# Performance work log

Hardware: AMD Instinct MI355X
Metric: run time of the kernel (lower is better)

The kernel has to match this reference:

```python
import jax, jax.numpy as jnp
import numpy as np

N, E = 50000, 800000
DIN, DH, DOUT = 128, 128, 64


def setup_inputs() -> dict:
    key = jax.random.key(0)
    ks = jax.random.split(key, 18)
    s = 0.05
    inp = {
        "x": jax.random.normal(ks[0], (N, DIN), dtype=jnp.float32),
        "edge_index": jax.random.randint(ks[1], (2, E), 0, N, dtype=jnp.int64),
        # conv1 MLP: Linear(DIN,DH), Linear(DH,DH)
        "c1_w1": jax.random.normal(ks[2], (DIN, DH), dtype=jnp.float32) * s,
        "c1_b1": jax.random.normal(ks[3], (DH,), dtype=jnp.float32) * s,
        "c1_w2": jax.random.normal(ks[4], (DH, DH), dtype=jnp.float32) * s,
        "c1_b2": jax.random.normal(ks[5], (DH,), dtype=jnp.float32) * s,
        # conv2 MLP
        "c2_w1": jax.random.normal(ks[6], (DH, DH), dtype=jnp.float32) * s,
        "c2_b1": jax.random.normal(ks[7], (DH,), dtype=jnp.float32) * s,
        "c2_w2": jax.random.normal(ks[8], (DH, DH), dtype=jnp.float32) * s,
        "c2_b2": jax.random.normal(ks[9], (DH,), dtype=jnp.float32) * s,
        # conv3 MLP
        "c3_w1": jax.random.normal(ks[10], (DH, DH), dtype=jnp.float32) * s,
        "c3_b1": jax.random.normal(ks[11], (DH,), dtype=jnp.float32) * s,
        "c3_w2": jax.random.normal(ks[12], (DH, DH), dtype=jnp.float32) * s,
        "c3_b2": jax.random.normal(ks[13], (DH,), dtype=jnp.float32) * s,
        # output head
        "lin1_w": jax.random.normal(ks[14], (DH, DH), dtype=jnp.float32) * s,
        "lin1_b": jax.random.normal(ks[15], (DH,), dtype=jnp.float32) * s,
        "lin2_w": jax.random.normal(ks[16], (DH, DOUT), dtype=jnp.float32) * s,
        "lin2_b": jax.random.normal(ks[17], (DOUT,), dtype=jnp.float32) * s,
    }
    return inp


def _gin_conv(h, src, dst, w1, b1, w2, b2):
    # PyG GINConv, eps=0: MLP((1+eps)*x + sum_{j->i} x_j)
    agg = jax.ops.segment_sum(h[src], dst, num_segments=h.shape[0])  # [N, D]
    z = h + agg
    z = jax.nn.relu(z @ w1 + b1)
    return jax.nn.relu(z @ w2 + b2)


def reference(x, edge_index, c1_w1, c1_b1, c1_w2, c1_b2,
              c2_w1, c2_b1, c2_w2, c2_b2,
              c3_w1, c3_b1, c3_w2, c3_b2,
              lin1_w, lin1_b, lin2_w, lin2_b):
    src, dst = edge_index[0], edge_index[1]
    h = _gin_conv(x, src, dst, c1_w1, c1_b1, c1_w2, c1_b2)
    h = jax.nn.relu(h)  # redundant after MLP ReLU, but faithful to source
    h = _gin_conv(h, src, dst, c2_w1, c2_b1, c2_w2, c2_b2)
    h = jax.nn.relu(h)
    h = _gin_conv(h, src, dst, c3_w1, c3_b1, c3_w2, c3_b2)
    h = jax.nn.relu(h @ lin1_w + lin1_b)
    return h @ lin2_w + lin2_b  # [N, DOUT]
```

## Files before the change

### kernel.cpp

```cpp
#include <hip/hip_runtime.h>
#include <hip/hip_bf16.h>

typedef __attribute__((ext_vector_type(8))) short bf16x8;
typedef __attribute__((ext_vector_type(4))) float f32x4;

#define DH 128
#define DOUT 64

static __device__ __forceinline__ unsigned short f2bf(float f) {
    __hip_bfloat16 h = __float2bfloat16(f);
    return *(unsigned short*)&h;
}
static __device__ __forceinline__ void accI(float& a0, float& a1, unsigned u, float s) {
    int lo = (int)(signed char)(u & 0xffu);
    int hi = (int)(signed char)(u >> 8);
    a0 += s * (float)lo;
    a1 += s * (float)hi;
}


struct WPrep {
    const float* src[8];
    unsigned short* dst[8];
};

__global__ void prep_conv_kernel(const float* __restrict__ x,
                                 char* __restrict__ xq, float* __restrict__ sx,
                                 char* __restrict__ hAq, float* __restrict__ sA,
                                 char* __restrict__ hBq, float* __restrict__ sB,
                                 int nA, WPrep p,
                                 int* __restrict__ cnt, int* __restrict__ rank,
                                 const int* __restrict__ dstv, int E, int N_) {
    int id = blockIdx.x * blockDim.x + threadIdx.x;
    if (id < nA) {
        float4 v = ((const float4*)x)[id];
        float m = fmaxf(fmaxf(fabsf(v.x), fabsf(v.y)), fmaxf(fabsf(v.z), fabsf(v.w)));
#pragma unroll
        for (int d = 16; d >= 1; d >>= 1) m = fmaxf(m, __shfl_xor(m, d));
        float inv = m > 0.f ? 127.f / m : 0.f;
        int q0 = __float2int_rn(v.x * inv);
        int q1 = __float2int_rn(v.y * inv);
        int q2 = __float2int_rn(v.z * inv);
        int q3 = __float2int_rn(v.w * inv);
        unsigned pk = (q0 & 0xff) | ((q1 & 0xff) << 8) | ((q2 & 0xff) << 16) | ((q3 & 0xff) << 24);
        ((unsigned*)xq)[id] = pk;
        if ((id & 31) == 0) sx[id >> 5] = m * (1.f / 127.f);
        return;
    }
    id -= nA;
    if (id < 7 * 16384 + 8192) {
        int m, off;
        if (id < 7 * 16384) { m = id >> 14; off = id & 16383; }
        else { m = 7; off = id - 7 * 16384; }
        int shift = (m == 7) ? 6 : 7;
        int nc = 1 << shift;
        int k = off >> shift;
        int n = off & (nc - 1);
        p.dst[m][n * 128 + k] = f2bf(p.src[m][off]);
        return;
    }
    id -= 7 * 16384 + 8192;
    if (id < 96) {
        int w = id >> 5, j = id & 31;
        unsigned* dst = (unsigned*)(w == 0 ? xq : (w == 1 ? hAq : hBq));
        dst[(size_t)N_ * 32 + j] = 0u;
        return;
    }
    id -= 96;
    if (id < 3) {
        (id == 0 ? sx : (id == 1 ? sA : sB))[N_] = 0.f;
        return;
    }
    id -= 3;
    if (id < E) {
        int d = dstv[id];
        if ((unsigned)d < (unsigned)N_) rank[id] = atomicAdd(&cnt[d], 1);
    }
}


__global__ void scan1_kernel(const int* __restrict__ cnt, int* __restrict__ rp_part,
                             int* __restrict__ bsum, int n) {
    __shared__ int s[256];
    int tid = threadIdx.x;
    int i = blockIdx.x * 256 + tid;
    int v = (i < n) ? ((cnt[i] + 7) & ~7) : 0;
    s[tid] = v;
    __syncthreads();
    for (int off = 1; off < 256; off <<= 1) {
        int t = (tid >= off) ? s[tid - off] : 0;
        __syncthreads();
        s[tid] += t;
        __syncthreads();
    }
    if (i <= n) rp_part[i] = s[tid] - v;
    if (tid == 255) bsum[blockIdx.x] = s[255];
}

__global__ void scan2_kernel(int* __restrict__ bsum, int nb) {
    __shared__ int s[256];
    int tid = threadIdx.x;
    int v = (tid < nb) ? bsum[tid] : 0;
    s[tid] = v;
    __syncthreads();
    for (int off = 1; off < 256; off <<= 1) {
        int t = (tid >= off) ? s[tid - off] : 0;
        __syncthreads();
        s[tid] += t;
        __syncthreads();
    }
    if (tid < nb) bsum[tid] = s[tid] - v;
}

__global__ void scan3_fill_kernel(const int* __restrict__ rp_part, const int* __restrict__ bsum,
                                  int* __restrict__ row_ptr,
                                  const int* __restrict__ src, const int* __restrict__ dst,
                                  const int* __restrict__ rank, const int* __restrict__ cnt,
                                  unsigned short* __restrict__ esrc,
                                  int n, int E) {
    int gid = blockIdx.x * blockDim.x + threadIdx.x;
    if (gid <= n) row_ptr[gid] = rp_part[gid] + bsum[gid >> 8];
    if (gid < n) {
        int st = rp_part[gid] + bsum[gid >> 8];
        int c = cnt[gid];
        int pe = (c + 7) & ~7;
        for (int j = c; j < pe; ++j) esrc[st + j] = (unsigned short)n;
    }
    if (gid < E) {
        int d = dst[gid];
        if ((unsigned)d < (unsigned)n)
            esrc[rp_part[d] + bsum[d >> 8] + rank[gid]] = (unsigned short)src[gid];
    }
}


template <bool HEAD>
__launch_bounds__(256, 6)
__global__ void layer_kernel(const char* __restrict__ hq, const float* __restrict__ sIn,
                             const int* __restrict__ rp,
                             const unsigned short* __restrict__ esrc,
                             const unsigned short* __restrict__ W1t,
                             const float* __restrict__ b1,
                             const unsigned short* __restrict__ W2t,
                             const float* __restrict__ b2,
                             const unsigned short* __restrict__ W3t,
                             const float* __restrict__ b3,
                             const unsigned short* __restrict__ W4t,
                             const float* __restrict__ b4,
                             char* __restrict__ outq, float* __restrict__ outs,
                             float* __restrict__ outp, int M) {
    constexpr int LDA = 128 + 8;
    constexpr int CAP = 1024;
    __shared__ __align__(16) unsigned short As[16][LDA];
    __shared__ __align__(16) unsigned short Zs[16][LDA];
    __shared__ __align__(16) int2 sIdx[CAP];

    int tid = threadIdx.x;
    int wave = __builtin_amdgcn_readfirstlane(tid >> 6);
    int lane = tid & 63;
    int row0 = blockIdx.x * 16;
    int nd0 = row0 + wave * 4;

    const char* hc = hq;
    unsigned voff = (unsigned)lane << 1;

    int wbv = rp[row0];
    int Cv = rp[min(row0 + 16, M)] - wbv;
    int wb = __builtin_amdgcn_readfirstlane(wbv);
    int C = __builtin_amdgcn_readfirstlane(Cv);

    int b[4], e[4];
#pragma unroll
    for (int i = 0; i < 4; ++i) {
        int ndc = min(nd0 + i, M);
        int nd1 = min(nd0 + i + 1, M);
        b[i] = rp[ndc] - wb;
        e[i] = rp[nd1] - wb;
    }

    float a0[4] = {0.f, 0.f, 0.f, 0.f}, a1[4] = {0.f, 0.f, 0.f, 0.f};

    for (int p0 = 0; p0 < C; p0 += CAP) {
        int cend = min(C, p0 + CAP);
        for (int i = tid; i < cend - p0; i += 256) {
            int id = esrc[wb + p0 + i];
            sIdx[i] = make_int2(id << 7, __float_as_int(sIn[id]));
        }
        __syncthreads();
#pragma unroll
        for (int i = 0; i < 4; ++i) {
            int nb = max(b[i], p0) - p0;
            int ne = min(e[i], cend) - p0;
            if (nb < ne) {
                int2 ia[8];
                unsigned ua[8];
#pragma unroll
                for (int t = 0; t < 8; ++t) ia[t] = sIdx[nb + t];
#pragma unroll
                for (int t = 0; t < 8; ++t)
                    ua[t] = *(const unsigned short*)(hc + (unsigned)ia[t].x + voff);
                for (int r = nb + 8; r < ne; r += 8) {
                    int2 ib[8];
                    unsigned ub[8];
#pragma unroll
                    for (int t = 0; t < 8; ++t) ib[t] = sIdx[r + t];
#pragma unroll
                    for (int t = 0; t < 8; ++t)
                        ub[t] = *(const unsigned short*)(hc + (unsigned)ib[t].x + voff);
#pragma unroll
                    for (int t = 0; t < 8; ++t) accI(a0[i], a1[i], ua[t], __int_as_float(ia[t].y));
#pragma unroll
                    for (int t = 0; t < 8; ++t) { ia[t] = ib[t]; ua[t] = ub[t]; }
                }
#pragma unroll
                for (int t = 0; t < 8; ++t) accI(a0[i], a1[i], ua[t], __int_as_float(ia[t].y));
            }
        }
        __syncthreads();
    }

#pragma unroll
    for (int i = 0; i < 4; ++i) {
        int ndc = min(nd0 + i, M);
        unsigned su = *(const unsigned short*)(hc + ((size_t)(unsigned)ndc << 7) + voff);
        accI(a0[i], a1[i], su, sIn[ndc]);
        unsigned pv = (unsigned)f2bf(a0[i]) | ((unsigned)f2bf(a1[i]) << 16);
        *(unsigned*)&As[wave * 4 + i][lane * 2] = pv;
    }
    __syncthreads();

    int quad = lane >> 4;
    int l16 = lane & 15;

    bf16x8 af[4];
#pragma unroll
    for (int kt = 0; kt < 4; ++kt)
        af[kt] = *(const bf16x8*)(&As[l16][kt * 32 + quad * 8]);
#pragma unroll
    for (int p = 0; p < 2; ++p) {
        int ncol = (wave * 2 + p) * 16 + l16;
        const unsigned short* wp = W1t + ncol * 128 + quad * 8;
        f32x4 a = {0.f, 0.f, 0.f, 0.f};
#pragma unroll
        for (int kt = 0; kt < 4; ++kt)
            a = __builtin_amdgcn_mfma_f32_16x16x32_bf16(
                af[kt], *(const bf16x8*)(wp + kt * 32), a, 0, 0, 0);
        float bs = b1[ncol];
#pragma unroll
        for (int r = 0; r < 4; ++r) {
            float v = a[r] + bs;
            if (v < 0.f) v = 0.f;
            Zs[quad * 4 + r][ncol] = f2bf(v);
        }
    }
    __syncthreads();

    bf16x8 zf[4];
#pragma unroll
    for (int kt = 0; kt < 4; ++kt)
        zf[kt] = *(const bf16x8*)(&Zs[l16][kt * 32 + quad * 8]);

    if (!HEAD) {
        __shared__ float Fs[16][132];
#pragma unroll
        for (int p = 0; p < 2; ++p) {
            int ncol = (wave * 2 + p) * 16 + l16;
            const unsigned short* wp = W2t + ncol * 128 + quad * 8;
            f32x4 a = {0.f, 0.f, 0.f, 0.f};
#pragma unroll
            for (int kt = 0; kt < 4; ++kt)
                a = __builtin_amdgcn_mfma_f32_16x16x32_bf16(
                    zf[kt], *(const bf16x8*)(wp + kt * 32), a, 0, 0, 0);
            float bs = b2[ncol];
#pragma unroll
            for (int r = 0; r < 4; ++r) {
                float v = a[r] + bs;
                if (v < 0.f) v = 0.f;
                Fs[quad * 4 + r][ncol] = v;
            }
        }
        __syncthreads();
        {
            int row = tid >> 4;
            int c0 = (tid & 15) * 8;
            float v8[8];
            float m = 0.f;
#pragma unroll
            for (int j = 0; j < 8; ++j) { v8[j] = Fs[row][c0 + j]; m = fmaxf(m, v8[j]); }
#pragma unroll
            for (int d = 8; d >= 1; d >>= 1) m = fmaxf(m, __shfl_xor(m, d));
            float inv = m > 0.f ? 127.f / m : 0.f;
            unsigned w0 = 0, w1 = 0;
#pragma unroll
            for (int j = 0; j < 4; ++j) {
                w0 |= (unsigned)(__float2int_rn(v8[j] * inv) & 0xff) << (8 * j);
                w1 |= (unsigned)(__float2int_rn(v8[4 + j] * inv) & 0xff) << (8 * j);
            }
            int grow = row0 + row;
            if (grow < M) {
                uint2 pk = make_uint2(w0, w1);
                ((uint2*)(outq + (size_t)grow * 128))[tid & 15] = pk;
                if ((tid & 15) == 0) outs[grow] = m * (1.f / 127.f);
            }
        }
    } else {
#pragma unroll
        for (int p = 0; p < 2; ++p) {
            int ncol = (wave * 2 + p) * 16 + l16;
            const unsigned short* wp = W2t + ncol * 128 + quad * 8;
            f32x4 a = {0.f, 0.f, 0.f, 0.f};
#pragma unroll
            for (int kt = 0; kt < 4; ++kt)
                a = __builtin_amdgcn_mfma_f32_16x16x32_bf16(
                    zf[kt], *(const bf16x8*)(wp + kt * 32), a, 0, 0, 0);
            float bs = b2[ncol];
#pragma unroll
            for (int r = 0; r < 4; ++r) {
                float v = a[r] + bs;
                if (v < 0.f) v = 0.f;
                As[quad * 4 + r][ncol] = f2bf(v);
            }
        }
        __syncthreads();
        bf16x8 hf[4];
#pragma unroll
        for (int kt = 0; kt < 4; ++kt)
            hf[kt] = *(const bf16x8*)(&As[l16][kt * 32 + quad * 8]);
#pragma unroll
        for (int p = 0; p < 2; ++p) {
            int ncol = (wave * 2 + p) * 16 + l16;
            const unsigned short* wp = W3t + ncol * 128 + quad * 8;
            f32x4 a = {0.f, 0.f, 0.f, 0.f};
#pragma unroll
            for (int kt = 0; kt < 4; ++kt)
                a = __builtin_amdgcn_mfma_f32_16x16x32_bf16(
                    hf[kt], *(const bf16x8*)(wp + kt * 32), a, 0, 0, 0);
            float bs = b3[ncol];
#pragma unroll
            for (int r = 0; r < 4; ++r) {
                float v = a[r] + bs;
                if (v < 0.f) v = 0.f;
                Zs[quad * 4 + r][ncol] = f2bf(v);
            }
        }
        __syncthreads();
        bf16x8 gf[4];
#pragma unroll
        for (int kt = 0; kt < 4; ++kt)
            gf[kt] = *(const bf16x8*)(&Zs[l16][kt * 32 + quad * 8]);
        {
            int ncol = wave * 16 + l16;
            const unsigned short* wp = W4t + ncol * 128 + quad * 8;
            f32x4 a = {0.f, 0.f, 0.f, 0.f};
#pragma unroll
            for (int kt = 0; kt < 4; ++kt)
                a = __builtin_amdgcn_mfma_f32_16x16x32_bf16(
                    gf[kt], *(const bf16x8*)(wp + kt * 32), a, 0, 0, 0);
            float bs = b4[ncol];
#pragma unroll
            for (int r = 0; r < 4; ++r) {
                int grow = row0 + quad * 4 + r;
                if (grow < M)
                    outp[(size_t)grow * 64 + ncol] = a[r] + bs;
            }
        }
    }
}


extern "C" void kernel_launch(void* const* d_in, const int* in_sizes, int n_in,
                              void* d_out, int out_size, void* d_ws, size_t ws_size,
                              hipStream_t stream) {
    const float* x = (const float*)d_in[0];
    const int* ei = (const int*)d_in[1];
    int N = in_sizes[0] / DH;
    int E = in_sizes[1] / 2;
    const int* src = ei;
    const int* dstv = ei + E;
    int Epad = E + 7 * N + 1024;

    char* ws = (char*)d_ws;
    size_t off = 0;
    auto alloc = [&](size_t bytes) -> void* {
        void* p = ws + off;
        off += (bytes + 255) & ~(size_t)255;
        return p;
    };
    char* xq  = (char*)alloc((size_t)(N + 1) * 128);
    char* hAq = (char*)alloc((size_t)(N + 1) * 128);
    char* hBq = (char*)alloc((size_t)(N + 1) * 128);
    float* sx = (float*)alloc((size_t)(N + 1) * 4);
    float* sA = (float*)alloc((size_t)(N + 1) * 4);
    float* sB = (float*)alloc((size_t)(N + 1) * 4);
    unsigned short* wt[8];
    for (int m = 0; m < 8; ++m) wt[m] = (unsigned short*)alloc(16384 * 2);
    int* cnt     = (int*)alloc((size_t)N * 4);
    int* rp_part = (int*)alloc((size_t)(N + 1) * 4);
    int* row_ptr = (int*)alloc((size_t)(N + 1) * 4);
    int* rank    = (int*)alloc((size_t)E * 4);
    int* bsum    = (int*)alloc(256 * 4);
    unsigned short* esrc = (unsigned short*)alloc((size_t)Epad * 2);

    WPrep wp;
    wp.src[0] = (const float*)d_in[2];
    wp.src[1] = (const float*)d_in[4];
    wp.src[2] = (const float*)d_in[6];
    wp.src[3] = (const float*)d_in[8];
    wp.src[4] = (const float*)d_in[10];
    wp.src[5] = (const float*)d_in[12];
    wp.src[6] = (const float*)d_in[14];
    wp.src[7] = (const float*)d_in[16];
    for (int m = 0; m < 8; ++m) wp.dst[m] = wt[m];

    hipMemsetAsync(cnt, 0, (size_t)N * 4, stream);

    int nA = N * 32;
    int conv_items = nA + 7 * 16384 + 8192 + 99 + E;
    prep_conv_kernel<<<(conv_items + 255) / 256, 256, 0, stream>>>(
        x, xq, sx, hAq, sA, hBq, sB, nA, wp, cnt, rank, dstv, E, N);

    int nb = (N + 1 + 255) / 256;
    int eb = (E + 255) / 256;
    scan1_kernel<<<nb, 256, 0, stream>>>(cnt, rp_part, bsum, N);
    scan2_kernel<<<1, 256, 0, stream>>>(bsum, nb);
    scan3_fill_kernel<<<eb, 256, 0, stream>>>(rp_part, bsum, row_ptr,
                                              src, dstv, rank, cnt, esrc, N, E);

    int gb = (N + 15) / 16;

    const float* c1b1 = (const float*)d_in[3];
    const float* c1b2 = (const float*)d_in[5];
    const float* c2b1 = (const float*)d_in[7];
    const float* c2b2 = (const float*)d_in[9];
    const float* c3b1 = (const float*)d_in[11];
    const float* c3b2 = (const float*)d_in[13];
    const float* l1b  = (const float*)d_in[15];
    const float* l2b  = (const float*)d_in[17];

    layer_kernel<false><<<gb, 256, 0, stream>>>(
        xq, sx, row_ptr, esrc, wt[0], c1b1, wt[1], c1b2,
        nullptr, nullptr, nullptr, nullptr, hAq, sA, nullptr, N);
    layer_kernel<false><<<gb, 256, 0, stream>>>(
        hAq, sA, row_ptr, esrc, wt[2], c2b1, wt[3], c2b2,
        nullptr, nullptr, nullptr, nullptr, hBq, sB, nullptr, N);
    layer_kernel<true><<<gb, 256, 0, stream>>>(
        hBq, sB, row_ptr, esrc, wt[4], c3b1, wt[5], c3b2,
        wt[6], l1b, wt[7], l2b, nullptr, nullptr, (float*)d_out, N);
}
```

Measured before the change: 311.1 us.

## Replace CSR build with per-block destination bins sorted in LDS

After: 335.8 us. 1.08x slower.

```diff
diff --git a/kernel.cpp b/kernel.cpp
--- a/kernel.cpp
+++ b/kernel.cpp
@@ -6,6 +6,7 @@
 
 #define DH 128
 #define DOUT 64
+#define BINCAP 1024
 
 static __device__ __forceinline__ unsigned short f2bf(float f) {
     __hip_bfloat16 h = __float2bfloat16(f);
@@ -29,8 +30,9 @@
                                  char* __restrict__ hAq, float* __restrict__ sA,
                                  char* __restrict__ hBq, float* __restrict__ sB,
                                  int nA, WPrep p,
-                                 int* __restrict__ cnt, int* __restrict__ rank,
-                                 const int* __restrict__ dstv, int E, int N_) {
+                                 int* __restrict__ bcnt, unsigned* __restrict__ binbuf,
+                                 const int* __restrict__ srcv, const int* __restrict__ dstv,
+                                 int E, int N_) {
     int id = blockIdx.x * blockDim.x + threadIdx.x;
     if (id < nA) {
         float4 v = ((const float4*)x)[id];
@@ -74,62 +76,13 @@
     id -= 3;
     if (id < E) {
         int d = dstv[id];
-        if ((unsigned)d < (unsigned)N_) rank[id] = atomicAdd(&cnt[d], 1);
-    }
-}
-
-
-__global__ void scan1_kernel(const int* __restrict__ cnt, int* __restrict__ rp_part,
-                             int* __restrict__ bsum, int n) {
-    __shared__ int s[256];
-    int tid = threadIdx.x;
-    int i = blockIdx.x * 256 + tid;
-    int v = (i < n) ? ((cnt[i] + 7) & ~7) : 0;
-    s[tid] = v;
-    __syncthreads();
-    for (int off = 1; off < 256; off <<= 1) {
-        int t = (tid >= off) ? s[tid - off] : 0;
-        __syncthreads();
-        s[tid] += t;
-        __syncthreads();
-    }
-    if (i <= n) rp_part[i] = s[tid] - v;
-    if (tid == 255) bsum[blockIdx.x] = s[255];
-}
-
-__global__ void scan2_kernel(int* __restrict__ bsum, int nb) {
-    __shared__ int s[256];
-    int tid = threadIdx.x;
-    int v = (tid < nb) ? bsum[tid] : 0;
-    s[tid] = v;
-    __syncthreads();
-    for (int off = 1; off < 256; off <<= 1) {
-        int t = (tid >= off) ? s[tid - off] : 0;
-        __syncthreads();
-        s[tid] += t;
-        __syncthreads();
-    }
-    if (tid < nb) bsum[tid] = s[tid] - v;
-}
-
-__global__ void scan3_fill_kernel(const int* __restrict__ rp_part, const int* __restrict__ bsum,
-                                  int* __restrict__ row_ptr,
-                                  const int* __restrict__ src, const int* __restrict__ dst,
-                                  const int* __restrict__ rank, const int* __restrict__ cnt,
-                                  unsigned short* __restrict__ esrc,
-                                  int n, int E) {
-    int gid = blockIdx.x * blockDim.x + threadIdx.x;
-    if (gid <= n) row_ptr[gid] = rp_part[gid] + bsum[gid >> 8];
-    if (gid < n) {
-        int st = rp_part[gid] + bsum[gid >> 8];
-        int c = cnt[gid];
-        int pe = (c + 7) & ~7;
-        for (int j = c; j < pe; ++j) esrc[st + j] = (unsigned short)n;
-    }
-    if (gid < E) {
-        int d = dst[gid];
-        if ((unsigned)d < (unsigned)n)
-            esrc[rp_part[d] + bsum[d >> 8] + rank[gid]] = (unsigned short)src[gid];
+        if ((unsigned)d < (unsigned)N_) {
+            int bin = d >> 4;
+            int pos = atomicAdd(&bcnt[bin], 1);
+            if (pos < BINCAP)
+                binbuf[(size_t)bin * BINCAP + pos] =
+                    (unsigned)srcv[id] | ((unsigned)(d & 15) << 16);
+        }
     }
 }
 
@@ -137,8 +90,7 @@
 template <bool HEAD>
 __launch_bounds__(256, 6)
 __global__ void layer_kernel(const char* __restrict__ hq, const float* __restrict__ sIn,
-                             const int* __restrict__ rp,
-                             const unsigned short* __restrict__ esrc,
+                             const int* __restrict__ bcnt, const unsigned* __restrict__ binbuf,
                              const unsigned short* __restrict__ W1t,
                              const float* __restrict__ b1,
                              const unsigned short* __restrict__ W2t,
@@ -150,10 +102,11 @@
                              char* __restrict__ outq, float* __restrict__ outs,
                              float* __restrict__ outp, int M) {
     constexpr int LDA = 128 + 8;
-    constexpr int CAP = 1024;
+    constexpr int SCAP = BINCAP + 16 * 8;
     __shared__ __align__(16) unsigned short As[16][LDA];
     __shared__ __align__(16) unsigned short Zs[16][LDA];
-    __shared__ __align__(16) int2 sIdx[CAP];
+    __shared__ __align__(16) int2 sIdx[SCAP];
+    __shared__ int nS[16], nE[16], nCur[16], CtotS;
 
     int tid = threadIdx.x;
     int wave = __builtin_amdgcn_readfirstlane(tid >> 6);
@@ -164,60 +117,77 @@
     const char* hc = hq;
     unsigned voff = (unsigned)lane << 1;
 
-    int wbv = rp[row0];
-    int Cv = rp[min(row0 + 16, M)] - wbv;
-    int wb = __builtin_amdgcn_readfirstlane(wbv);
-    int C = __builtin_amdgcn_readfirstlane(Cv);
+    int bin = blockIdx.x;
+    int C0 = min(bcnt[bin], BINCAP);
+    const unsigned* bb = binbuf + (size_t)bin * BINCAP;
+    if (tid < 16) nS[tid] = 0;
+    __syncthreads();
+    for (int i = tid; i < C0; i += 256) atomicAdd(&nS[(bb[i] >> 16) & 15], 1);
+    __syncthreads();
+    if (tid == 0) {
+        int acc = 0;
+#pragma unroll
+        for (int k = 0; k < 16; ++k) {
+            int c = nS[k];
+            nS[k] = acc; nCur[k] = acc;
+            acc += (c + 7) & ~7;
+            nE[k] = acc;
+        }
+        CtotS = acc;
+    }
+    __syncthreads();
+    int Ctot = __builtin_amdgcn_readfirstlane(CtotS);
+    int2 zent = make_int2(M << 7, 0);
+    for (int i = tid; i < Ctot; i += 256) sIdx[i] = zent;
+    __syncthreads();
+    for (int i = tid; i < C0; i += 256) {
+        unsigned ev = bb[i];
+        int node = (ev >> 16) & 15;
+        int pos = atomicAdd(&nCur[node], 1);
+        int idn = ev & 0xffff;
+        sIdx[pos] = make_int2(idn << 7, __float_as_int(sIn[idn]));
+    }
+    __syncthreads();
 
     int b[4], e[4];
 #pragma unroll
     for (int i = 0; i < 4; ++i) {
-        int ndc = min(nd0 + i, M);
-        int nd1 = min(nd0 + i + 1, M);
-        b[i] = rp[ndc] - wb;
-        e[i] = rp[nd1] - wb;
+        b[i] = __builtin_amdgcn_readfirstlane(nS[wave * 4 + i]);
+        e[i] = __builtin_amdgcn_readfirstlane(nE[wave * 4 + i]);
     }
 
     float a0[4] = {0.f, 0.f, 0.f, 0.f}, a1[4] = {0.f, 0.f, 0.f, 0.f};
 
-    for (int p0 = 0; p0 < C; p0 += CAP) {
-        int cend = min(C, p0 + CAP);
-        for (int i = tid; i < cend - p0; i += 256) {
-            int id = esrc[wb + p0 + i];
-            sIdx[i] = make_int2(id << 7, __float_as_int(sIn[id]));
-        }
-        __syncthreads();
-#pragma unroll
-        for (int i = 0; i < 4; ++i) {
-            int nb = max(b[i], p0) - p0;
-            int ne = min(e[i], cend) - p0;
-            if (nb < ne) {
-                int2 ia[8];
-                unsigned ua[8];
-#pragma unroll
-                for (int t = 0; t < 8; ++t) ia[t] = sIdx[nb + t];
+#pragma unroll
+    for (int i = 0; i < 4; ++i) {
+        int nb = b[i];
+        int ne = e[i];
+        if (nb < ne) {
+            int2 ia[8];
+            unsigned ua[8];
+#pragma unroll
+            for (int t = 0; t < 8; ++t) ia[t] = sIdx[nb + t];
+#pragma unroll
+            for (int t = 0; t < 8; ++t)
+                ua[t] = *(const unsigned short*)(hc + (unsigned)ia[t].x + voff);
+            for (int r = nb + 8; r < ne; r += 8) {
+                int2 ib[8];
+                unsigned ub[8];
+#pragma unroll
+                for (int t = 0; t < 8; ++t) ib[t] = sIdx[r + t];
 #pragma unroll
                 for (int t = 0; t < 8; ++t)
-                    ua[t] = *(const unsigned short*)(hc + (unsigned)ia[t].x + voff);
-                for (int r = nb + 8; r < ne; r += 8) {
-                    int2 ib[8];
-                    unsigned ub[8];
-#pragma unroll
-                    for (int t = 0; t < 8; ++t) ib[t] = sIdx[r + t];
-#pragma unroll
-                    for (int t = 0; t < 8; ++t)
-                        ub[t] = *(const unsigned short*)(hc + (unsigned)ib[t].x + voff);
-#pragma unroll
-                    for (int t = 0; t < 8; ++t) accI(a0[i], a1[i], ua[t], __int_as_float(ia[t].y));
-#pragma unroll
-                    for (int t = 0; t < 8; ++t) { ia[t] = ib[t]; ua[t] = ub[t]; }
-                }
+                    ub[t] = *(const unsigned short*)(hc + (unsigned)ib[t].x + voff);
 #pragma unroll
                 for (int t = 0; t < 8; ++t) accI(a0[i], a1[i], ua[t], __int_as_float(ia[t].y));
-            }
-        }
-        __syncthreads();
-    }
+#pragma unroll
+                for (int t = 0; t < 8; ++t) { ia[t] = ib[t]; ua[t] = ub[t]; }
+            }
+#pragma unroll
+            for (int t = 0; t < 8; ++t) accI(a0[i], a1[i], ua[t], __int_as_float(ia[t].y));
+        }
+    }
+    __syncthreads();
 
 #pragma unroll
     for (int i = 0; i < 4; ++i) {
@@ -377,7 +347,7 @@
     int E = in_sizes[1] / 2;
     const int* src = ei;
     const int* dstv = ei + E;
-    int Epad = E + 7 * N + 1024;
+    int nbins = (N + 15) / 16;
 
     char* ws = (char*)d_ws;
     size_t off = 0;
@@ -394,12 +364,8 @@
     float* sB = (float*)alloc((size_t)(N + 1) * 4);
     unsigned short* wt[8];
     for (int m = 0; m < 8; ++m) wt[m] = (unsigned short*)alloc(16384 * 2);
-    int* cnt     = (int*)alloc((size_t)N * 4);
-    int* rp_part = (int*)alloc((size_t)(N + 1) * 4);
-    int* row_ptr = (int*)alloc((size_t)(N + 1) * 4);
-    int* rank    = (int*)alloc((size_t)E * 4);
-    int* bsum    = (int*)alloc(256 * 4);
-    unsigned short* esrc = (unsigned short*)alloc((size_t)Epad * 2);
+    int* bcnt        = (int*)alloc((size_t)nbins * 4);
+    unsigned* binbuf = (unsigned*)alloc((size_t)nbins * BINCAP * 4);
 
     WPrep wp;
     wp.src[0] = (const float*)d_in[2];
@@ -412,21 +378,14 @@
     wp.src[7] = (const float*)d_in[16];
     for (int m = 0; m < 8; ++m) wp.dst[m] = wt[m];
 
-    hipMemsetAsync(cnt, 0, (size_t)N * 4, stream);
+    hipMemsetAsync(bcnt, 0, (size_t)nbins * 4, stream);
 
     int nA = N * 32;
     int conv_items = nA + 7 * 16384 + 8192 + 99 + E;
     prep_conv_kernel<<<(conv_items + 255) / 256, 256, 0, stream>>>(
-        x, xq, sx, hAq, sA, hBq, sB, nA, wp, cnt, rank, dstv, E, N);
-
-    int nb = (N + 1 + 255) / 256;
-    int eb = (E + 255) / 256;
-    scan1_kernel<<<nb, 256, 0, stream>>>(cnt, rp_part, bsum, N);
-    scan2_kernel<<<1, 256, 0, stream>>>(bsum, nb);
-    scan3_fill_kernel<<<eb, 256, 0, stream>>>(rp_part, bsum, row_ptr,
-                                              src, dstv, rank, cnt, esrc, N, E);
-
-    int gb = (N + 15) / 16;
+        x, xq, sx, hAq, sA, hBq, sB, nA, wp, bcnt, binbuf, src, dstv, E, N);
+
+    int gb = nbins;
 
     const float* c1b1 = (const float*)d_in[3];
     const float* c1b2 = (const float*)d_in[5];
@@ -438,12 +397,12 @@
     const float* l2b  = (const float*)d_in[17];
 
     layer_kernel<false><<<gb, 256, 0, stream>>>(
-        xq, sx, row_ptr, esrc, wt[0], c1b1, wt[1], c1b2,
+        xq, sx, bcnt, binbuf, wt[0], c1b1, wt[1], c1b2,
         nullptr, nullptr, nullptr, nullptr, hAq, sA, nullptr, N);
     layer_kernel<false><<<gb, 256, 0, stream>>>(
-        hAq, sA, row_ptr, esrc, wt[2], c2b1, wt[3], c2b2,
+        hAq, sA, bcnt, binbuf, wt[2], c2b1, wt[3], c2b2,
         nullptr, nullptr, nullptr, nullptr, hBq, sB, nullptr, N);
     layer_kernel<true><<<gb, 256, 0, stream>>>(
-        hBq, sB, row_ptr, esrc, wt[4], c3b1, wt[5], c3b2,
+        hBq, sB, bcnt, binbuf, wt[4], c3b1, wt[5], c3b2,
         wt[6], l1b, wt[7], l2b, nullptr, nullptr, (float*)d_out, N);
 }
```
